# Kernel optimization log

Hardware: AMD Instinct MI355X
Metric: run time of the kernel (lower is better)

The kernel has to match this reference:

```python
import jax, jax.numpy as jnp
import numpy as np

K = 10  # hardcoded top-k in the original forward


def setup_inputs() -> dict:
    key = jax.random.key(0)
    ks = jax.random.split(key, 7)
    B, F, N = 192, 256, 512
    stdv = 1.0 / np.sqrt(F)
    return {
        "v": jax.random.normal(ks[0], (B, F, N), dtype=jnp.float32),
        "g_w": jax.random.normal(ks[1], (F, F), dtype=jnp.float32) * stdv,  # Conv1d k=1 weight [out,in]
        "g_b": jax.random.normal(ks[2], (F,), dtype=jnp.float32) * stdv,
        "w1": jax.random.uniform(ks[3], (F, F), jnp.float32, -stdv, stdv),
        "b1": jax.random.uniform(ks[4], (F,), jnp.float32, -stdv, stdv),
        "w2": jax.random.uniform(ks[5], (F, F), jnp.float32, -stdv, stdv),
        "b2": jax.random.uniform(ks[6], (F,), jnp.float32, -stdv, stdv),
    }


def reference(v, g_w, g_b, w1, b1, w2, b2):
    B, Fdim, N = v.shape
    # g: Conv1d(k=1) then permute -> [B, N, nhid]
    g_v = jnp.einsum('bfn,hf->bnh', v, g_w) + g_b
    # affinity A = v^T v : [B, N, N]
    A = jnp.einsum('bfn,bfm->bnm', v, v)
    # top-K sparsification: keep only top-K entries per row
    _, idx = jax.lax.top_k(A, K)  # [B, N, K]
    b_i = jnp.arange(B)[:, None, None]
    n_i = jnp.arange(N)[None, :, None]
    keep = jnp.zeros(A.shape, dtype=bool).at[b_i, n_i, idx].set(True)
    A = jnp.where(keep, A, jnp.zeros((), A.dtype))
    # add self loops
    A = A + jnp.eye(N, dtype=A.dtype)
    # D^-0.5 A D^-0.5 (diagonal scaling, equivalent to diag_embed matmuls)
    deg = jnp.sum(A, axis=-1)  # [B, N]
    d = deg ** -0.5
    d = jnp.where(jnp.isinf(d), jnp.zeros((), d.dtype), d)
    A_hat = d[:, :, None] * A * d[:, None, :]
    # GCN layer 1: relu(A_hat @ (g_v @ w1) + b1)  (dropout p=0 -> identity)
    x = jax.nn.relu(jnp.einsum('bnm,bmh->bnh', A_hat, g_v @ w1) + b1)
    # GCN layer 2
    x = jnp.einsum('bnm,bmh->bnh', A_hat, x @ w2) + b2
    # permute back and residual
    return jnp.transpose(x, (0, 2, 1)) + v
```

## Files before the change

kernel.cpp:

```cpp
#include <hip/hip_runtime.h>
#include <float.h>

#define F_DIM 256
#define N_DIM 512
#define B_DIM 192
#define K_TOP 10

typedef __attribute__((ext_vector_type(8))) short short8;
typedef __attribute__((ext_vector_type(4))) float f32x4;

__device__ inline unsigned short f2bf(float x) {
    unsigned u = __builtin_bit_cast(unsigned, x);
    return (unsigned short)((u + 0x7fffu + ((u >> 16) & 1u)) >> 16);
}

__global__ __launch_bounds__(256) void k_combine(const float* __restrict__ g_w,
                                                 const float* __restrict__ g_b,
                                                 const float* __restrict__ w1,
                                                 const float* __restrict__ w2,
                                                 unsigned short* __restrict__ Wt1,
                                                 float* __restrict__ bc,
                                                 unsigned short* __restrict__ W2t) {
    const int j = threadIdx.x;
    const int bx = blockIdx.x;
    if (bx < F_DIM) {
        float acc = 0.f;
        for (int h = 0; h < F_DIM; ++h) acc += g_w[h * F_DIM + bx] * w1[h * F_DIM + j];
        Wt1[j * F_DIM + bx] = f2bf(acc);
    } else if (bx == F_DIM) {
        float acc = 0.f;
        for (int h = 0; h < F_DIM; ++h) acc += g_b[h] * w1[h * F_DIM + j];
        bc[j] = acc;
    } else {
        int f = bx - F_DIM - 1;
        W2t[j * F_DIM + f] = f2bf(w2[f * F_DIM + j]);
    }
}

__global__ __launch_bounds__(256) void k_to_bf16t(const float* __restrict__ v,
                                                  unsigned short* __restrict__ vt) {
    __shared__ float tile[32][33];
    const int b = blockIdx.z;
    const int n0 = blockIdx.x * 32;
    const int f0 = blockIdx.y * 32;
    const int tx = threadIdx.x & 31, ty = threadIdx.x >> 5;
    const float* vb = v + (size_t)b * F_DIM * N_DIM;
#pragma unroll
    for (int q = 0; q < 4; ++q)
        tile[ty + q * 8][tx] = vb[(size_t)(f0 + ty + q * 8) * N_DIM + n0 + tx];
    __syncthreads();
    const int wn = threadIdx.x >> 4;
    const int wf = threadIdx.x & 15;
    unsigned* vt32 = (unsigned*)vt;
#pragma unroll
    for (int q2 = 0; q2 < 2; ++q2) {
        int row = wn + q2 * 16;
        unsigned lo = f2bf(tile[wf * 2][row]);
        unsigned hi = f2bf(tile[wf * 2 + 1][row]);
        vt32[(size_t)(b * N_DIM + n0 + row) * (F_DIM / 2) + (f0 >> 1) + wf] = lo | (hi << 16);
    }
}

__global__ __launch_bounds__(256, 2) void k_topk_reg(const unsigned short* __restrict__ vt,
                                                     float* __restrict__ deg,
                                                     int* __restrict__ idxb,
                                                     float* __restrict__ wb) {
    __shared__ unsigned short stage[2][N_DIM * 32];

    const int lid = blockIdx.y * 8 + blockIdx.x;
    const int slot = lid >> 3;
    const int b = (lid & 7) + 8 * (slot >> 3);
    const int nblk = slot & 7;

    const int w = threadIdx.x >> 6;
    const int l = threadIdx.x & 63;
    const int l15 = l & 15;
    const int g = l >> 4;
    const int n0w = nblk * 64 + w * 16;
    const unsigned short* vtb = vt + (size_t)b * N_DIM * F_DIM;

    short8 bf[8];
#pragma unroll
    for (int s = 0; s < 8; ++s)
        bf[s] = *(const short8*)(vtb + (size_t)(n0w + l15) * F_DIM + s * 32 + g * 8);

    f32x4 acc[32];
#pragma unroll
    for (int mt = 0; mt < 32; ++mt) acc[mt] = (f32x4){0.f, 0.f, 0.f, 0.f};

#define STAGE(c, bufi)                                                           \
    {                                                                            \
        _Pragma("unroll")                                                        \
        for (int k = 0; k < 8; ++k) {                                            \
            int sid = w * 512 + k * 64 + l;                                      \
            int row = sid >> 2;                                                  \
            int sl = sid & 3;                                                    \
            const unsigned short* src = vtb + (size_t)row * F_DIM + (c) * 32 +   \
                                        ((sl ^ ((row >> 1) & 3)) << 3);          \
            __builtin_amdgcn_global_load_lds(                                    \
                (const __attribute__((address_space(1))) void*)src,              \
                (__attribute__((address_space(3))) void*)(                       \
                    (char*)&stage[bufi][0] + (size_t)(w * 512 + k * 64) * 16),   \
                16, 0, 0);                                                       \
        }                                                                        \
    }

    STAGE(0, 0);
    asm volatile("s_waitcnt vmcnt(0)" ::: "memory");
    __syncthreads();

    const int slx = g ^ ((l15 >> 1) & 3);
    for (int c = 0; c < 8; ++c) {
        const int cur = c & 1;
        if (c < 7) STAGE(c + 1, cur ^ 1);
        const char* sb = (const char*)&stage[cur][0];
        short8 bcur = bf[c];
#pragma unroll
        for (int mt = 0; mt < 32; ++mt) {
            const int row = mt * 16 + l15;
            short8 a = *(const short8*)(sb + row * 64 + (slx << 4));
            acc[mt] = __builtin_amdgcn_mfma_f32_16x16x32_bf16(a, bcur, acc[mt], 0, 0, 0);
        }
        asm volatile("s_waitcnt vmcnt(0)" ::: "memory");
        __syncthreads();
    }
#undef STAGE

    const int row = b * N_DIM + n0w + l15;
    float sum = 0.f;
    for (int it = 0; it < K_TOP; ++it) {
        float chv[4]; int che[4];
#pragma unroll
        for (int c = 0; c < 4; ++c) {
            float tv[16]; int te[16];
#pragma unroll
            for (int p = 0; p < 16; ++p) {
                const int e0 = c * 32 + 2 * p, e1 = e0 + 1;
                float a = acc[e0 >> 2][e0 & 3];
                float bb2 = acc[e1 >> 2][e1 & 3];
                bool tk = bb2 > a;
                tv[p] = tk ? bb2 : a;
                te[p] = tk ? e1 : e0;
            }
#pragma unroll
            for (int len = 8; len >= 1; len >>= 1) {
#pragma unroll
                for (int i2 = 0; i2 < 8; ++i2) {
                    if (i2 < len) {
                        bool tk = tv[i2 + len] > tv[i2];
                        tv[i2] = tk ? tv[i2 + len] : tv[i2];
                        te[i2] = tk ? te[i2 + len] : te[i2];
                    }
                }
            }
            chv[c] = tv[0]; che[c] = te[0];
        }
        bool t1 = chv[1] > chv[0];
        float m0 = t1 ? chv[1] : chv[0]; int ea = t1 ? che[1] : che[0];
        bool t2 = chv[3] > chv[2];
        float m1 = t2 ? chv[3] : chv[2]; int eb = t2 ? che[3] : che[2];
        bool t3 = m1 > m0;
        float bv = t3 ? m1 : m0; int be = t3 ? eb : ea;
        int bm = ((be >> 2) << 4) | (g << 2) | (be & 3);

#pragma unroll
        for (int off = 16; off <= 32; off <<= 1) {
            float ov = __shfl_xor(bv, off, 64);
            int om = __shfl_xor(bm, off, 64);
            if (ov > bv || (ov == bv && om < bm)) { bv = ov; bm = om; }
        }
        sum += bv;
        if (l < 16) {
            idxb[row * K_TOP + it] = bm;
            wb[row * (K_TOP + 1) + it] = bv;
        }
        if (it < K_TOP - 1) {
            int eo = ((bm >> 4) << 2) | (bm & 3);
            eo = (((bm >> 2) & 3) == g) ? eo : 999;
#pragma unroll
            for (int e = 0; e < 128; ++e)
                acc[e >> 2][e & 3] = (e == eo) ? -FLT_MAX : acc[e >> 2][e & 3];
        }
    }
    if (l < 16) deg[row] = sum + 1.0f;
}

__global__ __launch_bounds__(256) void k_scale(const float* __restrict__ deg,
                                               const int* __restrict__ idxb,
                                               const float* __restrict__ wb,
                                               float* __restrict__ wbs) {
    const int row = blockIdx.x * 256 + threadIdx.x;
    const float dg = deg[row];
    const float dn = (dg == 0.f) ? 0.f : 1.f / sqrtf(dg);
    const int bb = (row >> 9) << 9;
#pragma unroll
    for (int i = 0; i < K_TOP; ++i) {
        int m = idxb[row * K_TOP + i];
        float dgm = deg[bb + m];
        float dm = (dgm == 0.f) ? 0.f : 1.f / sqrtf(dgm);
        wbs[row * 12 + i] = dn * wb[row * (K_TOP + 1) + i] * dm;
    }
    wbs[row * 12 + K_TOP] = dn * dn;
}

template <bool ADD_BIAS>
__global__ __launch_bounds__(256, 2) void k_gemm_mfma(const unsigned short* __restrict__ At,
                                                      const unsigned short* __restrict__ Wt,
                                                      const float* __restrict__ bias,
                                                      float* __restrict__ C) {
    const int b = blockIdx.y;
    const int w = threadIdx.x >> 6;
    const int l = threadIdx.x & 63;
    const int l15 = l & 15;
    const int g = l >> 4;
    const int n0w = blockIdx.x * 128 + w * 32;
    const unsigned short* Ab = At + (size_t)b * N_DIM * F_DIM;

    f32x4 acc0[16], acc1[16];
#pragma unroll
    for (int jt = 0; jt < 16; ++jt) {
        acc0[jt] = (f32x4){0.f, 0.f, 0.f, 0.f};
        acc1[jt] = (f32x4){0.f, 0.f, 0.f, 0.f};
    }

    for (int s = 0; s < 8; ++s) {
        short8 a0 = *(const short8*)(Ab + (size_t)(n0w + l15) * F_DIM + s * 32 + g * 8);
        short8 a1 = *(const short8*)(Ab + (size_t)(n0w + 16 + l15) * F_DIM + s * 32 + g * 8);
#pragma unroll
        for (int jt = 0; jt < 16; ++jt) {
            short8 bf = *(const short8*)(Wt + (size_t)(jt * 16 + l15) * F_DIM + s * 32 + g * 8);
            acc0[jt] = __builtin_amdgcn_mfma_f32_16x16x32_bf16(a0, bf, acc0[jt], 0, 0, 0);
            acc1[jt] = __builtin_amdgcn_mfma_f32_16x16x32_bf16(a1, bf, acc1[jt], 0, 0, 0);
        }
    }

#pragma unroll
    for (int jt = 0; jt < 16; ++jt) {
        float bv = ADD_BIAS ? bias[jt * 16 + l15] : 0.f;
#pragma unroll
        for (int q = 0; q < 4; ++q) {
            int r0 = n0w + g * 4 + q;
            C[((size_t)b * N_DIM + r0) * F_DIM + jt * 16 + l15] = acc0[jt][q] + bv;
            int r1 = n0w + 16 + g * 4 + q;
            C[((size_t)b * N_DIM + r1) * F_DIM + jt * 16 + l15] = acc1[jt][q] + bv;
        }
    }
}

__global__ __launch_bounds__(256) void k_spmm_bf16(const float* __restrict__ X,
                                                   const int* __restrict__ idxb,
                                                   const float* __restrict__ wbs,
                                                   const float* __restrict__ bias,
                                                   unsigned short* __restrict__ Y) {
    const int lid = blockIdx.x;
    const int slot = lid >> 3;
    const int b = (lid & 7) + 8 * (slot >> 7);
    const int rowblk = slot & 127;
    const int w = threadIdx.x >> 6;
    const int l = threadIdx.x & 63;
    const int row = b * N_DIM + rowblk * 4 + w;

    const float* Xb = X + ((size_t)b << 9) * F_DIM;
    const int* id = idxb + row * K_TOP;
    const float* ww = wbs + (size_t)row * 12;

    float4 bv = ((const float4*)bias)[l];
    float4 xv = ((const float4*)(X + (size_t)row * F_DIM))[l];
    const float ws = ww[K_TOP];
    float4 acc;
    acc.x = ws * xv.x + bv.x; acc.y = ws * xv.y + bv.y;
    acc.z = ws * xv.z + bv.z; acc.w = ws * xv.w + bv.w;
#pragma unroll
    for (int i = 0; i < K_TOP; ++i) {
        float wi = ww[i];
        float4 gv = ((const float4*)(Xb + ((size_t)id[i] << 8)))[l];
        acc.x += wi * gv.x; acc.y += wi * gv.y;
        acc.z += wi * gv.z; acc.w += wi * gv.w;
    }
    acc.x = fmaxf(acc.x, 0.f); acc.y = fmaxf(acc.y, 0.f);
    acc.z = fmaxf(acc.z, 0.f); acc.w = fmaxf(acc.w, 0.f);
    uint2 p;
    p.x = (unsigned)f2bf(acc.x) | ((unsigned)f2bf(acc.y) << 16);
    p.y = (unsigned)f2bf(acc.z) | ((unsigned)f2bf(acc.w) << 16);
    ((uint2*)Y)[(size_t)row * (F_DIM / 4) + l] = p;
}

__global__ __launch_bounds__(256) void k_spmm_trans(const float* __restrict__ X,
                                                    const int* __restrict__ idxb,
                                                    const float* __restrict__ wbs,
                                                    const float* __restrict__ bias,
                                                    const float* __restrict__ v,
                                                    float* __restrict__ out) {
    __shared__ float tile[16][132];
    const int lid = blockIdx.x;
    const int slot = lid >> 3;
    const int b = (lid & 7) + 8 * (slot >> 6);
    const int tl = slot & 63;
    const int n0 = (tl & 31) * 16;
    const int f0 = (tl >> 5) * 128;
    const int w = threadIdx.x >> 6;
    const int l = threadIdx.x & 63;

    const float* Xb = X + ((size_t)b << 9) * F_DIM;
    const int rl = l >> 5;
    const int fq = l & 31;
    float4 bv = ((const float4*)bias)[(f0 >> 2) + fq];

    for (int p2 = 0; p2 < 2; ++p2) {
        const int rloc = p2 * 8 + w * 2 + rl;
        const int row = b * N_DIM + n0 + rloc;
        const int* id = idxb + row * K_TOP;
        const float* ww = wbs + (size_t)row * 12;
        float4 xv = ((const float4*)(X + (size_t)row * F_DIM + f0))[fq];
        const float ws = ww[K_TOP];
        float4 acc;
        acc.x = ws * xv.x + bv.x; acc.y = ws * xv.y + bv.y;
        acc.z = ws * xv.z + bv.z; acc.w = ws * xv.w + bv.w;
#pragma unroll
        for (int i = 0; i < K_TOP; ++i) {
            float wi = ww[i];
            float4 gv = ((const float4*)(Xb + ((size_t)id[i] << 8) + f0))[fq];
            acc.x += wi * gv.x; acc.y += wi * gv.y;
            acc.z += wi * gv.z; acc.w += wi * gv.w;
        }
        tile[rloc][fq * 4 + 0] = acc.x;
        tile[rloc][fq * 4 + 1] = acc.y;
        tile[rloc][fq * 4 + 2] = acc.z;
        tile[rloc][fq * 4 + 3] = acc.w;
    }
    __syncthreads();

    const int i4 = l & 3, fj = l >> 2;
#pragma unroll
    for (int k = 0; k < 2; ++k) {
        const int fl = k * 64 + w * 16 + fj;
        const size_t vo = (size_t)b * F_DIM * N_DIM + (size_t)(f0 + fl) * N_DIM + n0;
        float4 vv = ((const float4*)(v + vo))[i4];
        float4 o;
        o.x = tile[i4 * 4 + 0][fl] + vv.x;
        o.y = tile[i4 * 4 + 1][fl] + vv.y;
        o.z = tile[i4 * 4 + 2][fl] + vv.z;
        o.w = tile[i4 * 4 + 3][fl] + vv.w;
        ((float4*)(out + vo))[i4] = o;
    }
}

extern "C" void kernel_launch(void* const* d_in, const int* in_sizes, int n_in,
                              void* d_out, int out_size, void* d_ws, size_t ws_size,
                              hipStream_t stream) {
    const float* v   = (const float*)d_in[0];
    const float* g_w = (const float*)d_in[1];
    const float* g_b = (const float*)d_in[2];
    const float* w1  = (const float*)d_in[3];
    const float* b1  = (const float*)d_in[4];
    const float* w2  = (const float*)d_in[5];
    const float* b2  = (const float*)d_in[6];
    float* out = (float*)d_out;

    const size_t S = (size_t)B_DIM * N_DIM * F_DIM;
    float* bufA = (float*)d_ws;
    float* bufB = bufA + S;
    float* bc   = bufB + S;
    float* deg  = bc + F_DIM;
    float* wb   = deg + (size_t)B_DIM * N_DIM;
    int*   idxb = (int*)(wb + (size_t)B_DIM * N_DIM * (K_TOP + 1));
    unsigned short* Wt1 = (unsigned short*)(idxb + (size_t)B_DIM * N_DIM * K_TOP);
    unsigned short* W2t = Wt1 + F_DIM * F_DIM;

    unsigned short* vt   = (unsigned short*)bufB;
    unsigned short* x1bf = (unsigned short*)bufB;
    float* wbs = bufB + S / 2;

    k_combine<<<dim3(2 * F_DIM + 2), 256, 0, stream>>>(g_w, g_b, w1, w2, Wt1, bc, W2t);
    k_to_bf16t<<<dim3(N_DIM / 32, F_DIM / 32, B_DIM), 256, 0, stream>>>(v, vt);
    k_topk_reg<<<dim3(N_DIM / 64, B_DIM), 256, 0, stream>>>(vt, deg, idxb, wb);
    k_scale<<<dim3(B_DIM * N_DIM / 256), 256, 0, stream>>>(deg, idxb, wb, wbs);
    k_gemm_mfma<true><<<dim3(N_DIM / 128, B_DIM), 256, 0, stream>>>(vt, Wt1, bc, bufA);
    k_spmm_bf16<<<dim3(B_DIM * N_DIM / 4), 256, 0, stream>>>(bufA, idxb, wbs, b1, x1bf);
    k_gemm_mfma<false><<<dim3(N_DIM / 128, B_DIM), 256, 0, stream>>>(x1bf, W2t, nullptr, bufA);
    k_spmm_trans<<<dim3(B_DIM * N_DIM / 16 * 2), 256, 0, stream>>>(bufA, idxb, wbs, b2, v, out);
}
```

Before: 462.4 us.

## Split top-k affinity work across waves by column range to raise occupancy

After: 455.6 us. About the same (-1.5%).

```diff
diff --git a/kernel.cpp b/kernel.cpp
--- a/kernel.cpp
+++ b/kernel.cpp
@@ -61,34 +61,33 @@
     }
 }
 
-__global__ __launch_bounds__(256, 2) void k_topk_reg(const unsigned short* __restrict__ vt,
+__global__ __launch_bounds__(256, 4) void k_topk_reg(const unsigned short* __restrict__ vt,
                                                      float* __restrict__ deg,
                                                      int* __restrict__ idxb,
                                                      float* __restrict__ wb) {
-    __shared__ unsigned short stage[2][N_DIM * 32];
-
-    const int lid = blockIdx.y * 8 + blockIdx.x;
+    __shared__ unsigned short stage[N_DIM * 32];
+    __shared__ uint2 scr[32][4];
+
+    const int lid = blockIdx.x;
     const int slot = lid >> 3;
-    const int b = (lid & 7) + 8 * (slot >> 3);
-    const int nblk = slot & 7;
+    const int b = (lid & 7) + 8 * (slot >> 4);
+    const int n0 = (slot & 15) * 32;
 
     const int w = threadIdx.x >> 6;
     const int l = threadIdx.x & 63;
     const int l15 = l & 15;
     const int g = l >> 4;
-    const int n0w = nblk * 64 + w * 16;
+    const int mbase = w * 128;
     const unsigned short* vtb = vt + (size_t)b * N_DIM * F_DIM;
 
-    short8 bf[8];
-#pragma unroll
-    for (int s = 0; s < 8; ++s)
-        bf[s] = *(const short8*)(vtb + (size_t)(n0w + l15) * F_DIM + s * 32 + g * 8);
-
-    f32x4 acc[32];
-#pragma unroll
-    for (int mt = 0; mt < 32; ++mt) acc[mt] = (f32x4){0.f, 0.f, 0.f, 0.f};
-
-#define STAGE(c, bufi)                                                           \
+    f32x4 acc[8][2];
+#pragma unroll
+    for (int mt = 0; mt < 8; ++mt) {
+        acc[mt][0] = (f32x4){0.f, 0.f, 0.f, 0.f};
+        acc[mt][1] = (f32x4){0.f, 0.f, 0.f, 0.f};
+    }
+
+#define STAGE(c)                                                                 \
     {                                                                            \
         _Pragma("unroll")                                                        \
         for (int k = 0; k < 8; ++k) {                                            \
@@ -100,44 +99,42 @@
             __builtin_amdgcn_global_load_lds(                                    \
                 (const __attribute__((address_space(1))) void*)src,              \
                 (__attribute__((address_space(3))) void*)(                       \
-                    (char*)&stage[bufi][0] + (size_t)(w * 512 + k * 64) * 16),   \
+                    (char*)&stage[0] + (size_t)sid * 16),                        \
                 16, 0, 0);                                                       \
         }                                                                        \
     }
 
-    STAGE(0, 0);
-    asm volatile("s_waitcnt vmcnt(0)" ::: "memory");
-    __syncthreads();
-
     const int slx = g ^ ((l15 >> 1) & 3);
     for (int c = 0; c < 8; ++c) {
-        const int cur = c & 1;
-        if (c < 7) STAGE(c + 1, cur ^ 1);
-        const char* sb = (const char*)&stage[cur][0];
-        short8 bcur = bf[c];
-#pragma unroll
-        for (int mt = 0; mt < 32; ++mt) {
-            const int row = mt * 16 + l15;
-            short8 a = *(const short8*)(sb + row * 64 + (slx << 4));
-            acc[mt] = __builtin_amdgcn_mfma_f32_16x16x32_bf16(a, bcur, acc[mt], 0, 0, 0);
-        }
+        STAGE(c);
         asm volatile("s_waitcnt vmcnt(0)" ::: "memory");
         __syncthreads();
+        const char* sb = (const char*)&stage[0];
+        short8 b0 = *(const short8*)(sb + (n0 + l15) * 64 + (slx << 4));
+        short8 b1 = *(const short8*)(sb + (n0 + 16 + l15) * 64 + (slx << 4));
+#pragma unroll
+        for (int mt = 0; mt < 8; ++mt) {
+            const int mrow = mbase + mt * 16 + l15;
+            short8 a = *(const short8*)(sb + mrow * 64 + (slx << 4));
+            acc[mt][0] = __builtin_amdgcn_mfma_f32_16x16x32_bf16(a, b0, acc[mt][0], 0, 0, 0);
+            acc[mt][1] = __builtin_amdgcn_mfma_f32_16x16x32_bf16(a, b1, acc[mt][1], 0, 0, 0);
+        }
+        __syncthreads();
     }
 #undef STAGE
 
-    const int row = b * N_DIM + n0w + l15;
-    float sum = 0.f;
+    const int grow0 = b * N_DIM + n0 + l15;
+    float sum0 = 0.f, sum1 = 0.f;
     for (int it = 0; it < K_TOP; ++it) {
-        float chv[4]; int che[4];
-#pragma unroll
-        for (int c = 0; c < 4; ++c) {
+        float cv[2]; int cm[2];
+#pragma unroll
+        for (int nt = 0; nt < 2; ++nt) {
             float tv[16]; int te[16];
 #pragma unroll
             for (int p = 0; p < 16; ++p) {
-                const int e0 = c * 32 + 2 * p, e1 = e0 + 1;
-                float a = acc[e0 >> 2][e0 & 3];
-                float bb2 = acc[e1 >> 2][e1 & 3];
+                const int e0 = 2 * p, e1 = 2 * p + 1;
+                float a = acc[e0 >> 2][nt][e0 & 3];
+                float bb2 = acc[e1 >> 2][nt][e1 & 3];
                 bool tk = bb2 > a;
                 tv[p] = tk ? bb2 : a;
                 te[p] = tk ? e1 : e0;
@@ -153,36 +150,65 @@
                     }
                 }
             }
-            chv[c] = tv[0]; che[c] = te[0];
-        }
-        bool t1 = chv[1] > chv[0];
-        float m0 = t1 ? chv[1] : chv[0]; int ea = t1 ? che[1] : che[0];
-        bool t2 = chv[3] > chv[2];
-        float m1 = t2 ? chv[3] : chv[2]; int eb = t2 ? che[3] : che[2];
-        bool t3 = m1 > m0;
-        float bv = t3 ? m1 : m0; int be = t3 ? eb : ea;
-        int bm = ((be >> 2) << 4) | (g << 2) | (be & 3);
-
+            cv[nt] = tv[0];
+            cm[nt] = mbase + ((te[0] >> 2) << 4) + (g << 2) + (te[0] & 3);
+        }
 #pragma unroll
         for (int off = 16; off <= 32; off <<= 1) {
-            float ov = __shfl_xor(bv, off, 64);
-            int om = __shfl_xor(bm, off, 64);
-            if (ov > bv || (ov == bv && om < bm)) { bv = ov; bm = om; }
-        }
-        sum += bv;
+#pragma unroll
+            for (int nt = 0; nt < 2; ++nt) {
+                float ov = __shfl_xor(cv[nt], off, 64);
+                int om = __shfl_xor(cm[nt], off, 64);
+                if (ov > cv[nt] || (ov == cv[nt] && om < cm[nt])) { cv[nt] = ov; cm[nt] = om; }
+            }
+        }
         if (l < 16) {
-            idxb[row * K_TOP + it] = bm;
-            wb[row * (K_TOP + 1) + it] = bv;
+            scr[l15][w] = make_uint2(__builtin_bit_cast(unsigned, cv[0]), (unsigned)cm[0]);
+            scr[16 + l15][w] = make_uint2(__builtin_bit_cast(unsigned, cv[1]), (unsigned)cm[1]);
+        }
+        __syncthreads();
+        float wv[2]; int wm[2];
+#pragma unroll
+        for (int nt = 0; nt < 2; ++nt) {
+            const uint2* sr = &scr[nt * 16 + l15][0];
+            uint4 q01 = *(const uint4*)&sr[0];
+            uint4 q23 = *(const uint4*)&sr[2];
+            float v0 = __builtin_bit_cast(float, q01.x); int m0 = (int)q01.y;
+            float v1 = __builtin_bit_cast(float, q01.z); int m1 = (int)q01.w;
+            float v2 = __builtin_bit_cast(float, q23.x); int m2 = (int)q23.y;
+            float v3 = __builtin_bit_cast(float, q23.z); int m3 = (int)q23.w;
+            bool t1 = (v1 > v0) || (v1 == v0 && m1 < m0);
+            float va = t1 ? v1 : v0; int ma = t1 ? m1 : m0;
+            bool t2 = (v3 > v2) || (v3 == v2 && m3 < m2);
+            float vb2 = t2 ? v3 : v2; int mb = t2 ? m3 : m2;
+            bool t3 = (vb2 > va) || (vb2 == va && mb < ma);
+            wv[nt] = t3 ? vb2 : va; wm[nt] = t3 ? mb : ma;
+        }
+        __syncthreads();
+        sum0 += wv[0]; sum1 += wv[1];
+        if (w == 0 && l < 16) {
+            idxb[grow0 * K_TOP + it] = wm[0];
+            wb[grow0 * (K_TOP + 1) + it] = wv[0];
+            idxb[(grow0 + 16) * K_TOP + it] = wm[1];
+            wb[(grow0 + 16) * (K_TOP + 1) + it] = wv[1];
         }
         if (it < K_TOP - 1) {
-            int eo = ((bm >> 4) << 2) | (bm & 3);
-            eo = (((bm >> 2) & 3) == g) ? eo : 999;
-#pragma unroll
-            for (int e = 0; e < 128; ++e)
-                acc[e >> 2][e & 3] = (e == eo) ? -FLT_MAX : acc[e >> 2][e & 3];
-        }
-    }
-    if (l < 16) deg[row] = sum + 1.0f;
+#pragma unroll
+            for (int nt = 0; nt < 2; ++nt) {
+                const int mwin = wm[nt];
+                const bool own = ((mwin >> 7) == w) && (((mwin >> 2) & 3) == g);
+                const int eo = (((mwin >> 4) & 7) << 2) | (mwin & 3);
+#pragma unroll
+                for (int ee = 0; ee < 32; ++ee)
+                    acc[ee >> 2][nt][ee & 3] =
+                        (own && ee == eo) ? -FLT_MAX : acc[ee >> 2][nt][ee & 3];
+            }
+        }
+    }
+    if (w == 0 && l < 16) {
+        deg[grow0] = sum0 + 1.0f;
+        deg[grow0 + 16] = sum1 + 1.0f;
+    }
 }
 
 __global__ __launch_bounds__(256) void k_scale(const float* __restrict__ deg,
@@ -373,7 +399,7 @@
 
     k_combine<<<dim3(2 * F_DIM + 2), 256, 0, stream>>>(g_w, g_b, w1, w2, Wt1, bc, W2t);
     k_to_bf16t<<<dim3(N_DIM / 32, F_DIM / 32, B_DIM), 256, 0, stream>>>(v, vt);
-    k_topk_reg<<<dim3(N_DIM / 64, B_DIM), 256, 0, stream>>>(vt, deg, idxb, wb);
+    k_topk_reg<<<dim3(B_DIM * (N_DIM / 32)), 256, 0, stream>>>(vt, deg, idxb, wb);
     k_scale<<<dim3(B_DIM * N_DIM / 256), 256, 0, stream>>>(deg, idxb, wb, wbs);
     k_gemm_mfma<true><<<dim3(N_DIM / 128, B_DIM), 256, 0, stream>>>(vt, Wt1, bc, bufA);
     k_spmm_bf16<<<dim3(B_DIM * N_DIM / 4), 256, 0, stream>>>(bufA, idxb, wbs, b1, x1bf);
```
